# Performance work log

Hardware: AMD Instinct MI355X
Metric: run time of the kernel (lower is better)

The kernel has to match this reference:

```python
import jax, jax.numpy as jnp
import numpy as np

B, P_ATT, F, E, D, A, O, V, L = 128, 36, 2048, 1024, 1024, 1024, 512, 10000, 20


def setup_inputs() -> dict:
    key = jax.random.key(0)
    ks = jax.random.split(key, 20)
    g = lambda i, shape, s=0.02: jax.random.normal(ks[i], shape, jnp.float32) * s
    return {
        "img_att": g(0, (B, P_ATT, F), 1.0),
        "img_fc": g(1, (B, 1, F), 1.0),
        "encoded_captions": jax.random.randint(ks[2], (B, L), 0, V),
        "caption_lengths": jax.random.randint(ks[3], (B, 1), 2, L + 1),
        "emb": jax.random.uniform(ks[4], (V, E), jnp.float32, -0.1, 0.1),
        "Wfa": g(5, (A, F)), "bfa": jnp.zeros((A,), jnp.float32),
        "Wd1": g(6, (A, D)), "bd1": jnp.zeros((A,), jnp.float32),
        "Wd2": g(7, (A, D)), "bd2": jnp.zeros((A,), jnp.float32),
        "Wfull": g(8, (1, A)), "bfull": jnp.zeros((1,), jnp.float32),
        "Wlang": g(9, (O, D)), "blang": jnp.zeros((O,), jnp.float32),
        "Watt": g(10, (O, D)), "batt": jnp.zeros((O,), jnp.float32),
        "Wout": g(11, (V, 2 * O)), "bout": jnp.zeros((V,), jnp.float32),
        "Wll_ih": g(12, (4 * D, E + D + F)), "Wll_hh": g(13, (4 * D, D)), "bll": jnp.zeros((4 * D,), jnp.float32),
        "Wal_ih": g(14, (4 * D, F)), "Wal_hh": g(15, (4 * D, D)), "bal": jnp.zeros((4 * D,), jnp.float32),
        "Wfc": g(16, (V, D)), "bfc": jnp.zeros((V,), jnp.float32),
    }


def _lstm_cell(x, h, c, Wih, Whh, b):
    # torch LSTMCell: gates ordered i, f, g, o; b = b_ih + b_hh
    gates = x @ Wih.T + h @ Whh.T + b
    i, f, g, o = jnp.split(gates, 4, axis=-1)
    c_new = jax.nn.sigmoid(f) * c + jax.nn.sigmoid(i) * jnp.tanh(g)
    h_new = jax.nn.sigmoid(o) * jnp.tanh(c_new)
    return h_new, c_new


def reference(img_att, img_fc, encoded_captions, caption_lengths, emb,
              Wfa, bfa, Wd1, bd1, Wd2, bd2, Wfull, bfull,
              Wlang, blang, Watt, batt, Wout, bout,
              Wll_ih, Wll_hh, bll, Wal_ih, Wal_hh, bal, Wfc, bfc):
    lengths = caption_lengths[:, 0]
    sort_ind = jnp.argsort(-lengths)  # stable descending sort by length
    lengths = lengths[sort_ind]
    image_features = jnp.concatenate([img_att, img_fc], axis=1)[sort_ind]  # (B, P, F)
    image_fc = img_fc[sort_ind, 0]  # (B, F)
    enc_caps = encoded_captions[sort_ind]
    embeddings = emb[enc_caps]  # (B, L, E)
    decode_lengths = lengths - 1
    T = enc_caps.shape[1] - 1
    Bsz = image_features.shape[0]
    Ddim = Wll_hh.shape[1]

    # attention key projection of image features is time-invariant: precompute
    att1 = jnp.einsum('bpf,af->bpa', image_features, Wfa) + bfa  # (B, P, A)

    def step(carry, x_t):
        h1, c1, h2, c2 = carry
        emb_t, t = x_t
        active = (t < decode_lengths)[:, None]  # (B, 1): rows beyond batch_size_t in torch
        x1 = jnp.concatenate([emb_t, h2, image_fc], axis=-1)
        h1n, c1n = _lstm_cell(x1, h1, c1, Wll_ih, Wll_hh, bll)
        preds1 = h1n @ Wfc.T + bfc  # dropout is identity in eval
        e = jax.nn.relu(att1 + (h1n @ Wd1.T + bd1)[:, None, :] + (h2 @ Wd2.T + bd2)[:, None, :])
        scores = jnp.einsum('bpa,a->bp', e, Wfull[0]) + bfull[0]
        alpha = jax.nn.softmax(scores, axis=1)
        awe = jnp.einsum('bpf,bp->bf', image_features, alpha)
        h2n, c2n = _lstm_cell(awe, h2, c2, Wal_ih, Wal_hh, bal)
        hid = jax.nn.relu(jnp.concatenate([h1n @ Wlang.T + blang, h2n @ Watt.T + batt], axis=-1))
        out = hid @ Wout.T + bout
        h1 = jnp.where(active, h1n, h1); c1 = jnp.where(active, c1n, c1)
        h2 = jnp.where(active, h2n, h2); c2 = jnp.where(active, c2n, c2)
        ys = (jnp.where(active, out, 0.0), jnp.where(active, preds1, 0.0), jnp.where(active, alpha, 0.0))
        return (h1, c1, h2, c2), ys

    init = tuple(jnp.zeros((Bsz, Ddim), image_features.dtype) for _ in range(4))
    xs = (jnp.swapaxes(embeddings[:, :T], 0, 1), jnp.arange(T))
    _, (preds, preds1, alphas) = jax.lax.scan(step, init, xs)
    predictions = jnp.swapaxes(preds, 0, 1)      # (B, T, V)
    predictions_1 = jnp.swapaxes(preds1, 0, 1)   # (B, T, V)
    alphas = jnp.swapaxes(alphas, 0, 1)          # (B, T, P)
    return predictions, predictions_1, enc_caps, decode_lengths, alphas, sort_ind
```

## Files before the change

### kernel.cpp

```cpp
#include <hip/hip_runtime.h>
#include <math.h>

#define BATCH 128
#define PATT 36
#define P_TOT 37
#define FDIM 2048
#define EDIM 1024
#define DDIM 1024
#define ADIM 1024
#define VOCAB 10000
#define LCAP 20
#define TSTEPS 19

typedef __attribute__((ext_vector_type(8))) short bf16x8v;
typedef __attribute__((ext_vector_type(4))) float f32x4v;

__device__ __forceinline__ ushort f2bf(float f) {
  unsigned u = __float_as_uint(f);
  unsigned r = (u + 0x7fffu + ((u >> 16) & 1u)) >> 16;
  return (ushort)r;
}
__device__ __forceinline__ float bf2f(ushort u) {
  return __uint_as_float(((unsigned)u) << 16);
}

__device__ __forceinline__ void gld16(const ushort* g, ushort* l) {
  __builtin_amdgcn_global_load_lds(
      (const __attribute__((address_space(1))) unsigned int*)(g),
      (__attribute__((address_space(3))) unsigned int*)(l), 16, 0, 0);
}

__global__ void setup_kernel(const int* __restrict__ cap_len,
                             const int* __restrict__ enc_caps,
                             int* __restrict__ sort_ind, int* __restrict__ dec_len,
                             float* __restrict__ out_enc, float* __restrict__ out_dec,
                             float* __restrict__ out_si) {
  __shared__ int s_len[BATCH];
  __shared__ int s_ind[BATCH];
  int tid = threadIdx.x;
  if (tid < BATCH) s_len[tid] = cap_len[tid];
  __syncthreads();
  if (tid < BATCH) {
    int key = s_len[tid];
    int pos = 0;
#pragma unroll 8
    for (int j = 0; j < BATCH; ++j) {
      int lj = s_len[j];
      pos += (lj > key) || (lj == key && j < tid);
    }
    s_ind[pos] = tid;
  }
  __syncthreads();
  for (int i = threadIdx.x; i < BATCH; i += blockDim.x) {
    int si = s_ind[i];
    sort_ind[i] = si;
    int dl = s_len[si] - 1;
    dec_len[i] = dl;
    out_dec[i] = (float)dl;
    out_si[i] = (float)si;
  }
  for (int i = threadIdx.x; i < BATCH * LCAP; i += blockDim.x) {
    int b = i / LCAP, l = i - b * LCAP;
    out_enc[i] = (float)enc_caps[s_ind[b] * LCAP + l];
  }
}

struct Seg { const float* src; ushort* dst; unsigned n; };
struct SegTab { Seg s[11]; };

__global__ __launch_bounds__(256) void convert_kernel(SegTab tab) {
  Seg sg = tab.s[blockIdx.y];
  unsigned i0 = (blockIdx.x * 256u + threadIdx.x) * 8u;
  if (i0 >= sg.n) return;
  float4 f0 = *(const float4*)(sg.src + i0);
  float4 f1 = *(const float4*)(sg.src + i0 + 4);
  ushort r[8];
  r[0] = f2bf(f0.x); r[1] = f2bf(f0.y); r[2] = f2bf(f0.z); r[3] = f2bf(f0.w);
  r[4] = f2bf(f1.x); r[5] = f2bf(f1.y); r[6] = f2bf(f1.z); r[7] = f2bf(f1.w);
  *(uint4*)(sg.dst + i0) = *(uint4*)r;
}

__global__ __launch_bounds__(256) void img_cat_kernel(const float* __restrict__ img_att,
                                                      const float* __restrict__ img_fc,
                                                      ushort* __restrict__ img_cat) {
  int b = blockIdx.x, p = blockIdx.y;
  const float* src = (p < PATT) ? img_att + ((size_t)b * PATT + p) * FDIM
                                : img_fc + (size_t)b * FDIM;
  ushort* dst = img_cat + ((size_t)b * P_TOT + p) * FDIM;
  int i0 = threadIdx.x * 8;
  float4 f0 = *(const float4*)(src + i0);
  float4 f1 = *(const float4*)(src + i0 + 4);
  ushort r[8];
  r[0] = f2bf(f0.x); r[1] = f2bf(f0.y); r[2] = f2bf(f0.z); r[3] = f2bf(f0.w);
  r[4] = f2bf(f1.x); r[5] = f2bf(f1.y); r[6] = f2bf(f1.z); r[7] = f2bf(f1.w);
  *(uint4*)(dst + i0) = *(uint4*)r;
}

__global__ __launch_bounds__(256) void gemm_mfma_kernel(
    const ushort* __restrict__ X, int ldx,
    const ushort* __restrict__ Wa, int Ka,
    const ushort* __restrict__ Wb, int Kb,
    const float* __restrict__ bias1, const float* __restrict__ bias2,
    float* __restrict__ C, ushort* __restrict__ Cb, long ldc,
    int N, int relu, const int* __restrict__ dec_len, int t)
{
  __shared__ __align__(16) ushort s_A[3][128][64];
  __shared__ __align__(16) ushort s_B[3][64][64];

  const int tid = threadIdx.x;
  const int lane = tid & 63;
  const int wv = tid >> 6;
  const int wm = wv >> 1;
  const int wn = wv & 1;
  const int q = lane >> 4;
  const int c16 = lane & 15;

  const int bm = blockIdx.x * 128;
  const int bn = blockIdx.y * 64;
  const int K = Ka + Kb;
  const int nt = K >> 6;

  f32x4v acc[4][2];
#pragma unroll
  for (int i = 0; i < 4; ++i)
#pragma unroll
    for (int j = 0; j < 2; ++j) acc[i][j] = (f32x4v){0.f, 0.f, 0.f, 0.f};

  auto stage = [&](int s, int tch) {
    const int k0 = tch << 6;
#pragma unroll
    for (int i = 0; i < 4; ++i) {
      int gid = i * 256 + tid;
      int r = gid >> 3, gp = gid & 7;
      int gl = gp ^ (r & 7);
      const ushort* src = X + (size_t)(bm + r) * ldx + k0 + gl * 8;
      gld16(src, &s_A[s][r][gp * 8]);
    }
#pragma unroll
    for (int i = 0; i < 2; ++i) {
      int gid = i * 256 + tid;
      int r = gid >> 3, gp = gid & 7;
      int gl = gp ^ (r & 7);
      int gn = bn + r;
      if (gn >= N) gn = N - 1;
      int kk = k0 + gl * 8;
      const ushort* src = (kk < Ka) ? Wa + (size_t)gn * Ka + kk
                                    : Wb + (size_t)gn * Kb + (kk - Ka);
      gld16(src, &s_B[s][r][gp * 8]);
    }
  };

  stage(0, 0);
  if (nt > 1) {
    stage(1, 1);
    asm volatile("s_waitcnt vmcnt(6)" ::: "memory");
  } else {
    asm volatile("s_waitcnt vmcnt(0)" ::: "memory");
  }
  __builtin_amdgcn_s_barrier();
  asm volatile("" ::: "memory");

  int cur = 0;
  for (int k = 0; k < nt; ++k) {
    if (k + 2 < nt) {
      int nxt = cur + 2; if (nxt >= 3) nxt -= 3;
      stage(nxt, k + 2);
    }
#pragma unroll
    for (int ks = 0; ks < 2; ++ks) {
      const int gpa = ((ks << 2) + q) ^ (c16 & 7);
      bf16x8v a[4], b[2];
#pragma unroll
      for (int mf = 0; mf < 4; ++mf)
        a[mf] = *(const bf16x8v*)&s_A[cur][wm * 64 + mf * 16 + c16][gpa * 8];
#pragma unroll
      for (int nf = 0; nf < 2; ++nf)
        b[nf] = *(const bf16x8v*)&s_B[cur][wn * 32 + nf * 16 + c16][gpa * 8];
#pragma unroll
      for (int mf = 0; mf < 4; ++mf)
#pragma unroll
        for (int nf = 0; nf < 2; ++nf)
          acc[mf][nf] = __builtin_amdgcn_mfma_f32_16x16x32_bf16(a[mf], b[nf], acc[mf][nf], 0, 0, 0);
    }
    if (k + 2 < nt) asm volatile("s_waitcnt vmcnt(6)" ::: "memory");
    else            asm volatile("s_waitcnt vmcnt(0)" ::: "memory");
    __builtin_amdgcn_s_barrier();
    asm volatile("" ::: "memory");
    cur = (cur == 2) ? 0 : cur + 1;
  }

#pragma unroll
  for (int nf = 0; nf < 2; ++nf) {
    int gcol = bn + wn * 32 + nf * 16 + c16;
    if (gcol >= N) continue;
    float bsum = bias1[gcol] + (bias2 ? bias2[gcol] : 0.f);
#pragma unroll
    for (int mf = 0; mf < 4; ++mf) {
#pragma unroll
      for (int rr = 0; rr < 4; ++rr) {
        int grow = bm + wm * 64 + mf * 16 + q * 4 + rr;
        float v = acc[mf][nf][rr] + bsum;
        if (relu) v = fmaxf(v, 0.f);
        if (dec_len && !(t < dec_len[grow])) v = 0.f;
        if (C)  C[(size_t)grow * ldc + gcol] = v;
        if (Cb) Cb[(size_t)grow * ldc + gcol] = f2bf(v);
      }
    }
  }
}

__global__ void build_x1_kernel(const float* __restrict__ emb, const int* __restrict__ enc_caps,
                                const int* __restrict__ sort_ind, const ushort* __restrict__ img_cat,
                                const ushort* __restrict__ h1bf, const ushort* __restrict__ h2bf,
                                ushort* __restrict__ x1cat, int t) {
  int b = blockIdx.x;
  int si = sort_ind[b];
  int cap = enc_caps[si * LCAP + t];
  const float* erow = emb + (size_t)cap * EDIM;
  const ushort* fcrow = img_cat + ((size_t)si * P_TOT + PATT) * FDIM;
  ushort* dst = x1cat + (size_t)b * 5120;
  for (int k = threadIdx.x; k < EDIM; k += 256) dst[k] = f2bf(erow[k]);
  for (int k = threadIdx.x; k < DDIM; k += 256) dst[EDIM + k] = h2bf[b * DDIM + k];
  for (int k = threadIdx.x; k < FDIM; k += 256) dst[EDIM + DDIM + k] = fcrow[k];
  for (int k = threadIdx.x; k < DDIM; k += 256) dst[EDIM + DDIM + FDIM + k] = h1bf[b * DDIM + k];
}

__global__ void lstm_cell_kernel(const float* __restrict__ gates,
                                 float* __restrict__ h, float* __restrict__ c,
                                 const int* __restrict__ dec_len, int t,
                                 ushort* __restrict__ hbf,
                                 ushort* __restrict__ hcat, const ushort* __restrict__ h_other_bf) {
  int idx = blockIdx.x * blockDim.x + threadIdx.x;
  int b = idx >> 10, j = idx & 1023;
  const float* g = gates + (size_t)b * 4096;
  float iv = 1.f / (1.f + expf(-g[j]));
  float fv = 1.f / (1.f + expf(-g[1024 + j]));
  float gv = tanhf(g[2048 + j]);
  float ov = 1.f / (1.f + expf(-g[3072 + j]));
  float cn = fv * c[idx] + iv * gv;
  float hn = ov * tanhf(cn);
  bool act = t < dec_len[b];
  float hw = act ? hn : h[idx];
  float cw = act ? cn : c[idx];
  h[idx] = hw; c[idx] = cw;
  hbf[idx] = f2bf(hw);
  if (hcat) {
    hcat[b * 2048 + j] = f2bf(hw);
    hcat[b * 2048 + 1024 + j] = h_other_bf[idx];
  }
}

__global__ __launch_bounds__(256) void attention_kernel(
    const ushort* __restrict__ att1, const float* __restrict__ d12,
    const float* __restrict__ Wfull, const float* __restrict__ bfull,
    const ushort* __restrict__ img_cat,
    const int* __restrict__ sort_ind, const int* __restrict__ dec_len,
    ushort* __restrict__ x2cat, const ushort* __restrict__ h2bf,
    float* __restrict__ out_alphas, int t) {
  int b = blockIdx.x;
  int si = sort_ind[b];
  __shared__ float dsh[ADIM];
  __shared__ float sc[P_TOT];
  __shared__ float al[P_TOT + 3];
  int tid = threadIdx.x;
  for (int k = tid; k < ADIM; k += 256) dsh[k] = d12[b * ADIM + k];
  __syncthreads();
  int wave = tid >> 6, lane = tid & 63;
  for (int p = wave; p < P_TOT; p += 4) {
    const ushort* arow = att1 + ((size_t)si * P_TOT + p) * ADIM;
    float s = 0.f;
    for (int k = lane * 4; k < ADIM; k += 256) {
      ushort4 av = *(const ushort4*)&arow[k];
      float e0 = fmaxf(bf2f(av.x) + dsh[k + 0], 0.f);
      float e1 = fmaxf(bf2f(av.y) + dsh[k + 1], 0.f);
      float e2 = fmaxf(bf2f(av.z) + dsh[k + 2], 0.f);
      float e3 = fmaxf(bf2f(av.w) + dsh[k + 3], 0.f);
      s += e0 * Wfull[k] + e1 * Wfull[k + 1] + e2 * Wfull[k + 2] + e3 * Wfull[k + 3];
    }
    for (int off = 32; off; off >>= 1) s += __shfl_down(s, off, 64);
    if (lane == 0) sc[p] = s + bfull[0];
  }
  __syncthreads();
  if (tid == 0) {
    float mx = sc[0];
    for (int p = 1; p < P_TOT; ++p) mx = fmaxf(mx, sc[p]);
    float sum = 0.f;
    for (int p = 0; p < P_TOT; ++p) { float e = expf(sc[p] - mx); al[p] = e; sum += e; }
    float inv = 1.f / sum;
    for (int p = 0; p < P_TOT; ++p) al[p] *= inv;
  }
  __syncthreads();
  bool act = t < dec_len[b];
  if (tid < P_TOT)
    out_alphas[((size_t)b * TSTEPS + t) * P_TOT + tid] = act ? al[tid] : 0.f;
  for (int f0 = tid * 4; f0 < FDIM; f0 += 1024) {
    float a0 = 0.f, a1 = 0.f, a2 = 0.f, a3 = 0.f;
#pragma unroll 4
    for (int p = 0; p < P_TOT; ++p) {
      ushort4 iv = *(const ushort4*)&img_cat[((size_t)si * P_TOT + p) * FDIM + f0];
      float w = al[p];
      a0 += w * bf2f(iv.x); a1 += w * bf2f(iv.y);
      a2 += w * bf2f(iv.z); a3 += w * bf2f(iv.w);
    }
    ushort* dst = x2cat + (size_t)b * 3072 + f0;
    dst[0] = f2bf(a0); dst[1] = f2bf(a1); dst[2] = f2bf(a2); dst[3] = f2bf(a3);
  }
  for (int j = tid; j < DDIM; j += 256)
    x2cat[(size_t)b * 3072 + FDIM + j] = h2bf[b * DDIM + j];
}

extern "C" void kernel_launch(void* const* d_in, const int* in_sizes, int n_in,
                              void* d_out, int out_size, void* d_ws, size_t ws_size,
                              hipStream_t stream) {
  const float* img_att = (const float*)d_in[0];
  const float* img_fc  = (const float*)d_in[1];
  const int*   enc_caps= (const int*)d_in[2];
  const int*   cap_len = (const int*)d_in[3];
  const float* emb     = (const float*)d_in[4];
  const float* Wfa     = (const float*)d_in[5];
  const float* bfa     = (const float*)d_in[6];
  const float* Wd1     = (const float*)d_in[7];
  const float* bd1     = (const float*)d_in[8];
  const float* Wd2     = (const float*)d_in[9];
  const float* bd2     = (const float*)d_in[10];
  const float* Wfull   = (const float*)d_in[11];
  const float* bfull   = (const float*)d_in[12];
  const float* Wlang   = (const float*)d_in[13];
  const float* blang   = (const float*)d_in[14];
  const float* Watt    = (const float*)d_in[15];
  const float* batt    = (const float*)d_in[16];
  const float* Wout    = (const float*)d_in[17];
  const float* bout    = (const float*)d_in[18];
  const float* Wll_ih  = (const float*)d_in[19];
  const float* Wll_hh  = (const float*)d_in[20];
  const float* bll     = (const float*)d_in[21];
  const float* Wal_ih  = (const float*)d_in[22];
  const float* Wal_hh  = (const float*)d_in[23];
  const float* bal     = (const float*)d_in[24];
  const float* Wfc     = (const float*)d_in[25];
  const float* bfc     = (const float*)d_in[26];

  int* sort_ind = (int*)d_ws;
  int* dec_len  = sort_ind + BATCH;
  float* fbase = (float*)d_ws + 256;
  const size_t BD = (size_t)BATCH * DDIM;
  float* h1    = fbase;
  float* c1    = h1 + BD;
  float* h2    = c1 + BD;
  float* c2    = h2 + BD;
  float* gates = c2 + BD;
  float* d12   = gates + (size_t)BATCH * 4096;
  ushort* ubase = (ushort*)(d12 + BD);
  ushort* h1bf   = ubase;
  ushort* h2bf   = h1bf + BD;
  ushort* x1cat  = h2bf + BD;
  ushort* hcat   = x1cat + (size_t)BATCH * 5120;
  ushort* x2cat  = hcat + (size_t)BATCH * 2048;
  ushort* hid_bf = x2cat + (size_t)BATCH * 3072;
  ushort* att1_bf= hid_bf + BD;
  ushort* img_cat= att1_bf + (size_t)BATCH * P_TOT * ADIM;
  ushort* wb     = img_cat + (size_t)BATCH * P_TOT * FDIM;
  ushort* Wfa_b  = wb;                 wb += (size_t)ADIM * FDIM;
  ushort* Wd1_b  = wb;                 wb += (size_t)ADIM * DDIM;
  ushort* Wd2_b  = wb;                 wb += (size_t)ADIM * DDIM;
  ushort* Wlang_b= wb;                 wb += (size_t)512 * DDIM;
  ushort* Watt_b = wb;                 wb += (size_t)512 * DDIM;
  ushort* Wout_b = wb;                 wb += (size_t)VOCAB * 1024;
  ushort* Wll_ih_b = wb;               wb += (size_t)4096 * 4096;
  ushort* Wll_hh_b = wb;               wb += (size_t)4096 * 1024;
  ushort* Wal_ih_b = wb;               wb += (size_t)4096 * 2048;
  ushort* Wal_hh_b = wb;               wb += (size_t)4096 * 1024;
  ushort* Wfc_b  = wb;                 wb += (size_t)VOCAB * 1024;

  float* out      = (float*)d_out;
  float* out_pred = out;
  float* out_pred1= out_pred  + (size_t)BATCH * TSTEPS * VOCAB;
  float* out_enc  = out_pred1 + (size_t)BATCH * TSTEPS * VOCAB;
  float* out_dec  = out_enc + (size_t)BATCH * LCAP;
  float* out_alph = out_dec + BATCH;
  float* out_si   = out_alph + (size_t)BATCH * TSTEPS * P_TOT;

  setup_kernel<<<1, 256, 0, stream>>>(cap_len, enc_caps, sort_ind, dec_len,
                                      out_enc, out_dec, out_si);
  hipMemsetAsync(h1, 0, 4 * BD * sizeof(float), stream);
  hipMemsetAsync(h1bf, 0, 2 * BD * sizeof(ushort), stream);

  SegTab tab;
  tab.s[0]  = {Wfa,    Wfa_b,    (unsigned)(ADIM * FDIM)};
  tab.s[1]  = {Wd1,    Wd1_b,    (unsigned)(ADIM * DDIM)};
  tab.s[2]  = {Wd2,    Wd2_b,    (unsigned)(ADIM * DDIM)};
  tab.s[3]  = {Wlang,  Wlang_b,  (unsigned)(512 * DDIM)};
  tab.s[4]  = {Watt,   Watt_b,   (unsigned)(512 * DDIM)};
  tab.s[5]  = {Wout,   Wout_b,   (unsigned)(VOCAB * 1024)};
  tab.s[6]  = {Wll_ih, Wll_ih_b, (unsigned)(4096 * 4096)};
  tab.s[7]  = {Wll_hh, Wll_hh_b, (unsigned)(4096 * 1024)};
  tab.s[8]  = {Wal_ih, Wal_ih_b, (unsigned)(4096 * 2048)};
  tab.s[9]  = {Wal_hh, Wal_hh_b, (unsigned)(4096 * 1024)};
  tab.s[10] = {Wfc,    Wfc_b,    (unsigned)(VOCAB * 1024)};
  convert_kernel<<<dim3(8192, 11), 256, 0, stream>>>(tab);

  img_cat_kernel<<<dim3(BATCH, P_TOT), 256, 0, stream>>>(img_att, img_fc, img_cat);

  gemm_mfma_kernel<<<dim3(37, 16), 256, 0, stream>>>(
      img_cat, FDIM, Wfa_b, FDIM, nullptr, 0, bfa, nullptr,
      nullptr, att1_bf, ADIM, ADIM, 0, nullptr, 0);

  const long ldo = (long)TSTEPS * VOCAB;
  for (int t = 0; t < TSTEPS; ++t) {
    build_x1_kernel<<<BATCH, 256, 0, stream>>>(emb, enc_caps, sort_ind, img_cat,
                                               h1bf, h2bf, x1cat, t);
    gemm_mfma_kernel<<<dim3(1, 64), 256, 0, stream>>>(
        x1cat, 5120, Wll_ih_b, 4096, Wll_hh_b, 1024, bll, nullptr,
        gates, nullptr, 4096, 4096, 0, nullptr, 0);
    lstm_cell_kernel<<<(BATCH * DDIM) / 256, 256, 0, stream>>>(
        gates, h1, c1, dec_len, t, h1bf, hcat, h2bf);
    gemm_mfma_kernel<<<dim3(1, 157), 256, 0, stream>>>(
        h1bf, 1024, Wfc_b, 1024, nullptr, 0, bfc, nullptr,
        out_pred1 + (size_t)t * VOCAB, nullptr, ldo, VOCAB, 0, dec_len, t);
    gemm_mfma_kernel<<<dim3(1, 16), 256, 0, stream>>>(
        hcat, 2048, Wd1_b, 1024, Wd2_b, 1024, bd1, bd2,
        d12, nullptr, 1024, 1024, 0, nullptr, 0);
    attention_kernel<<<BATCH, 256, 0, stream>>>(
        att1_bf, d12, Wfull, bfull, img_cat, sort_ind, dec_len,
        x2cat, h2bf, out_alph, t);
    gemm_mfma_kernel<<<dim3(1, 64), 256, 0, stream>>>(
        x2cat, 3072, Wal_ih_b, 2048, Wal_hh_b, 1024, bal, nullptr,
        gates, nullptr, 4096, 4096, 0, nullptr, 0);
    lstm_cell_kernel<<<(BATCH * DDIM) / 256, 256, 0, stream>>>(
        gates, h2, c2, dec_len, t, h2bf, nullptr, nullptr);
    gemm_mfma_kernel<<<dim3(1, 8), 256, 0, stream>>>(
        h1bf, 1024, Wlang_b, 1024, nullptr, 0, blang, nullptr,
        nullptr, hid_bf, 1024, 512, 1, nullptr, 0);
    gemm_mfma_kernel<<<dim3(1, 8), 256, 0, stream>>>(
        h2bf, 1024, Watt_b, 1024, nullptr, 0, batt, nullptr,
        nullptr, hid_bf + 512, 1024, 512, 1, nullptr, 0);
    gemm_mfma_kernel<<<dim3(1, 157), 256, 0, stream>>>(
        hid_bf, 1024, Wout_b, 1024, nullptr, 0, bout, nullptr,
        out_pred + (size_t)t * VOCAB, nullptr, ldo, VOCAB, 0, dec_len, t);
  }
}
```

Measured before the change: 5.498 ms.

## Fuse LSTM cell into gate GEMM epilogue and gather GEMM inputs directly

Fuses the LSTM cell into the gate GEMM epilogue by interleaving the i,f,g,o rows of the LSTM weights and biases, so each 64-column tile holds all four gates for 16 hidden units. The concat-building kernels are removed: the GEMM A-loader gathers rows straight from the embedding, h, image features and awe buffers through per-row base pointers. The h buffers are double-buffered, the Wlang and Watt GEMMs are merged into one launch, and the pipeline depth goes from three to four stages. This cuts kernel launches and intermediate gate and concat traffic per step, at the cost of more LDS and a more complex kernel.

```diff
diff --git a/kernel.cpp b/kernel.cpp
--- a/kernel.cpp
+++ b/kernel.cpp
@@ -30,11 +30,19 @@
       (__attribute__((address_space(3))) unsigned int*)(l), 16, 0, 0);
 }
 
+__device__ __forceinline__ void wait_stages(int cnt) {
+  if (cnt >= 2)      asm volatile("s_waitcnt vmcnt(12)" ::: "memory");
+  else if (cnt == 1) asm volatile("s_waitcnt vmcnt(6)"  ::: "memory");
+  else               asm volatile("s_waitcnt vmcnt(0)"  ::: "memory");
+}
+
 __global__ void setup_kernel(const int* __restrict__ cap_len,
                              const int* __restrict__ enc_caps,
                              int* __restrict__ sort_ind, int* __restrict__ dec_len,
                              float* __restrict__ out_enc, float* __restrict__ out_dec,
-                             float* __restrict__ out_si) {
+                             float* __restrict__ out_si,
+                             const float* __restrict__ bll, const float* __restrict__ bal,
+                             float* __restrict__ bll_p, float* __restrict__ bal_p) {
   __shared__ int s_len[BATCH];
   __shared__ int s_ind[BATCH];
   int tid = threadIdx.x;
@@ -51,7 +59,7 @@
     s_ind[pos] = tid;
   }
   __syncthreads();
-  for (int i = threadIdx.x; i < BATCH; i += blockDim.x) {
+  for (int i = tid; i < BATCH; i += blockDim.x) {
     int si = s_ind[i];
     sort_ind[i] = si;
     int dl = s_len[si] - 1;
@@ -59,14 +67,19 @@
     out_dec[i] = (float)dl;
     out_si[i] = (float)si;
   }
-  for (int i = threadIdx.x; i < BATCH * LCAP; i += blockDim.x) {
+  for (int i = tid; i < BATCH * LCAP; i += blockDim.x) {
     int b = i / LCAP, l = i - b * LCAP;
     out_enc[i] = (float)enc_caps[s_ind[b] * LCAP + l];
   }
-}
-
-struct Seg { const float* src; ushort* dst; unsigned n; };
-struct SegTab { Seg s[11]; };
+  for (int p = tid; p < 4096; p += blockDim.x) {
+    int src = (p & 3) * 1024 + (p >> 2);
+    bll_p[p] = bll[src];
+    bal_p[p] = bal[src];
+  }
+}
+
+struct Seg { const float* src; ushort* dst; unsigned n; unsigned rl; };
+struct SegTab { Seg s[12]; };
 
 __global__ __launch_bounds__(256) void convert_kernel(SegTab tab) {
   Seg sg = tab.s[blockIdx.y];
@@ -77,7 +90,13 @@
   ushort r[8];
   r[0] = f2bf(f0.x); r[1] = f2bf(f0.y); r[2] = f2bf(f0.z); r[3] = f2bf(f0.w);
   r[4] = f2bf(f1.x); r[5] = f2bf(f1.y); r[6] = f2bf(f1.z); r[7] = f2bf(f1.w);
-  *(uint4*)(sg.dst + i0) = *(uint4*)r;
+  unsigned dsti = i0;
+  if (sg.rl) {
+    unsigned rw = i0 >> sg.rl;
+    unsigned col = i0 & ((1u << sg.rl) - 1u);
+    dsti = ((4u * (rw & 1023u) + (rw >> 10)) << sg.rl) + col;
+  }
+  *(uint4*)(sg.dst + dsti) = *(uint4*)r;
 }
 
 __global__ __launch_bounds__(256) void img_cat_kernel(const float* __restrict__ img_att,
@@ -96,16 +115,38 @@
   *(uint4*)(dst + i0) = *(uint4*)r;
 }
 
+struct GatherX {
+  const ushort* p[4];
+  int kend[4];
+  int rstride[4];
+  int mode[4];
+  int nseg;
+};
+
 __global__ __launch_bounds__(256) void gemm_mfma_kernel(
-    const ushort* __restrict__ X, int ldx,
-    const ushort* __restrict__ Wa, int Ka,
+    const ushort* __restrict__ Xp, int ldx,
+    const ushort* __restrict__ Wap, int Ka,
     const ushort* __restrict__ Wb, int Kb,
-    const float* __restrict__ bias1, const float* __restrict__ bias2,
-    float* __restrict__ C, ushort* __restrict__ Cb, long ldc,
-    int N, int relu, const int* __restrict__ dec_len, int t)
+    const float* __restrict__ bias1p, const float* __restrict__ bias2,
+    float* __restrict__ C, ushort* __restrict__ Cbp, long ldc,
+    int N, int relu, const int* __restrict__ dec_len, int t,
+    GatherX gx, const int* __restrict__ sort_ind_g, const int* __restrict__ enc_caps_g,
+    float* __restrict__ lstm_h, float* __restrict__ lstm_c, ushort* __restrict__ lstm_hbf,
+    const ushort* __restrict__ Xalt, const ushort* __restrict__ Waalt,
+    const float* __restrict__ biasalt, ushort* __restrict__ Cbalt, int ysplit)
 {
-  __shared__ __align__(16) ushort s_A[3][128][64];
-  __shared__ __align__(16) ushort s_B[3][64][64];
+  __shared__ __align__(16) ushort s_A[4][128][64];
+  __shared__ __align__(16) ushort s_B[4][64][64];
+  __shared__ const ushort* s_rowbase[4][128];
+
+  const ushort* X = Xp;
+  const ushort* Wa = Wap;
+  const float* bias1 = bias1p;
+  ushort* Cb = Cbp;
+  int by = blockIdx.y;
+  if (ysplit && by >= ysplit) {
+    X = Xalt; Wa = Waalt; bias1 = biasalt; Cb = Cbalt; by -= ysplit;
+  }
 
   const int tid = threadIdx.x;
   const int lane = tid & 63;
@@ -116,9 +157,25 @@
   const int c16 = lane & 15;
 
   const int bm = blockIdx.x * 128;
-  const int bn = blockIdx.y * 64;
+  const int bn = by * 64;
   const int K = Ka + Kb;
   const int nt = K >> 6;
+  const bool gather = gx.nseg > 0;
+
+  if (gather) {
+    for (int r = tid; r < 128; r += 256) {
+      int si = sort_ind_g[r];
+      for (int sgi = 0; sgi < gx.nseg; ++sgi) {
+        const ushort* bp;
+        int m = gx.mode[sgi];
+        if (m == 0)      bp = gx.p[sgi] + (size_t)r * gx.rstride[sgi];
+        else if (m == 1) bp = gx.p[sgi] + (size_t)enc_caps_g[si * LCAP + t] * gx.rstride[sgi];
+        else             bp = gx.p[sgi] + ((size_t)si * P_TOT + PATT) * gx.rstride[sgi];
+        s_rowbase[sgi][r] = bp;
+      }
+    }
+    __syncthreads();
+  }
 
   f32x4v acc[4][2];
 #pragma unroll
@@ -128,19 +185,30 @@
 
   auto stage = [&](int s, int tch) {
     const int k0 = tch << 6;
-#pragma unroll
-    for (int i = 0; i < 4; ++i) {
-      int gid = i * 256 + tid;
-      int r = gid >> 3, gp = gid & 7;
-      int gl = gp ^ (r & 7);
-      const ushort* src = X + (size_t)(bm + r) * ldx + k0 + gl * 8;
-      gld16(src, &s_A[s][r][gp * 8]);
+    if (gather) {
+      int sg = 0;
+#pragma unroll
+      for (int z = 0; z < 3; ++z)
+        if (sg + 1 < gx.nseg && k0 >= gx.kend[sg]) ++sg;
+      const int kst = sg ? gx.kend[sg - 1] : 0;
+#pragma unroll
+      for (int i = 0; i < 4; ++i) {
+        int gid = i * 256 + tid;
+        int r = gid >> 3, gp = gid & 7, gl = gp ^ (r & 7);
+        gld16(s_rowbase[sg][r] + (k0 - kst) + gl * 8, &s_A[s][r][gp * 8]);
+      }
+    } else {
+#pragma unroll
+      for (int i = 0; i < 4; ++i) {
+        int gid = i * 256 + tid;
+        int r = gid >> 3, gp = gid & 7, gl = gp ^ (r & 7);
+        gld16(X + (size_t)(bm + r) * ldx + k0 + gl * 8, &s_A[s][r][gp * 8]);
+      }
     }
 #pragma unroll
     for (int i = 0; i < 2; ++i) {
       int gid = i * 256 + tid;
-      int r = gid >> 3, gp = gid & 7;
-      int gl = gp ^ (r & 7);
+      int r = gid >> 3, gp = gid & 7, gl = gp ^ (r & 7);
       int gn = bn + r;
       if (gn >= N) gn = N - 1;
       int kk = k0 + gl * 8;
@@ -150,43 +218,81 @@
     }
   };
 
-  stage(0, 0);
-  if (nt > 1) {
-    stage(1, 1);
-    asm volatile("s_waitcnt vmcnt(6)" ::: "memory");
-  } else {
-    asm volatile("s_waitcnt vmcnt(0)" ::: "memory");
-  }
+  auto compute = [&](int s) {
+#pragma unroll
+    for (int ks = 0; ks < 2; ++ks) {
+      const int gpa = ((ks << 2) + q) ^ (c16 & 7);
+      bf16x8v a[4], b2[2];
+#pragma unroll
+      for (int mf = 0; mf < 4; ++mf)
+        a[mf] = *(const bf16x8v*)&s_A[s][wm * 64 + mf * 16 + c16][gpa * 8];
+#pragma unroll
+      for (int nf = 0; nf < 2; ++nf)
+        b2[nf] = *(const bf16x8v*)&s_B[s][wn * 32 + nf * 16 + c16][gpa * 8];
+#pragma unroll
+      for (int mf = 0; mf < 4; ++mf)
+#pragma unroll
+        for (int nf = 0; nf < 2; ++nf)
+          acc[mf][nf] = __builtin_amdgcn_mfma_f32_16x16x32_bf16(a[mf], b2[nf], acc[mf][nf], 0, 0, 0);
+    }
+  };
+
+  const int pre = nt < 3 ? nt : 3;
+  for (int s2 = 0; s2 < pre; ++s2) stage(s2, s2);
+  wait_stages(pre - 1);
   __builtin_amdgcn_s_barrier();
   asm volatile("" ::: "memory");
 
-  int cur = 0;
   for (int k = 0; k < nt; ++k) {
-    if (k + 2 < nt) {
-      int nxt = cur + 2; if (nxt >= 3) nxt -= 3;
-      stage(nxt, k + 2);
-    }
-#pragma unroll
-    for (int ks = 0; ks < 2; ++ks) {
-      const int gpa = ((ks << 2) + q) ^ (c16 & 7);
-      bf16x8v a[4], b[2];
-#pragma unroll
-      for (int mf = 0; mf < 4; ++mf)
-        a[mf] = *(const bf16x8v*)&s_A[cur][wm * 64 + mf * 16 + c16][gpa * 8];
-#pragma unroll
-      for (int nf = 0; nf < 2; ++nf)
-        b[nf] = *(const bf16x8v*)&s_B[cur][wn * 32 + nf * 16 + c16][gpa * 8];
-#pragma unroll
-      for (int mf = 0; mf < 4; ++mf)
-#pragma unroll
-        for (int nf = 0; nf < 2; ++nf)
-          acc[mf][nf] = __builtin_amdgcn_mfma_f32_16x16x32_bf16(a[mf], b[nf], acc[mf][nf], 0, 0, 0);
-    }
-    if (k + 2 < nt) asm volatile("s_waitcnt vmcnt(6)" ::: "memory");
-    else            asm volatile("s_waitcnt vmcnt(0)" ::: "memory");
+    if (k + 3 < nt) stage((k + 3) & 3, k + 3);
+    compute(k & 3);
+    int li = (k + 3 < nt) ? (k + 3) : (nt - 1);
+    int cnt = li - (k + 1);
+    if (cnt < 0) cnt = 0;
+    wait_stages(cnt);
     __builtin_amdgcn_s_barrier();
     asm volatile("" ::: "memory");
-    cur = (cur == 2) ? 0 : cur + 1;
+  }
+
+  if (lstm_h) {
+    float* ft = (float*)&s_A[0][0][0];
+#pragma unroll
+    for (int nf = 0; nf < 2; ++nf) {
+      int lc = wn * 32 + nf * 16 + c16;
+      float bsum = bias1[bn + lc];
+#pragma unroll
+      for (int mf = 0; mf < 4; ++mf)
+#pragma unroll
+        for (int rr = 0; rr < 4; ++rr) {
+          int lr = wm * 64 + mf * 16 + q * 4 + rr;
+          ft[lr * 64 + lc] = acc[mf][nf][rr] + bsum;
+        }
+    }
+    __syncthreads();
+    const int j0 = bn >> 2;
+#pragma unroll
+    for (int uu = 0; uu < 8; ++uu) {
+      int u = uu * 256 + tid;
+      int b = u >> 4, jj = u & 15;
+      float gi_ = ft[b * 64 + jj * 4 + 0];
+      float gf_ = ft[b * 64 + jj * 4 + 1];
+      float gg_ = ft[b * 64 + jj * 4 + 2];
+      float go_ = ft[b * 64 + jj * 4 + 3];
+      float siv = 1.f / (1.f + expf(-gi_));
+      float sfv = 1.f / (1.f + expf(-gf_));
+      float sov = 1.f / (1.f + expf(-go_));
+      int idx = b * 1024 + j0 + jj;
+      float co = lstm_c[idx];
+      float cn = sfv * co + siv * tanhf(gg_);
+      float hn = sov * tanhf(cn);
+      bool act = t < dec_len[b];
+      float hw = act ? hn : lstm_h[idx];
+      float cw = act ? cn : co;
+      lstm_h[idx] = hw;
+      lstm_c[idx] = cw;
+      lstm_hbf[idx] = f2bf(hw);
+    }
+    return;
   }
 
 #pragma unroll
@@ -209,54 +315,12 @@
   }
 }
 
-__global__ void build_x1_kernel(const float* __restrict__ emb, const int* __restrict__ enc_caps,
-                                const int* __restrict__ sort_ind, const ushort* __restrict__ img_cat,
-                                const ushort* __restrict__ h1bf, const ushort* __restrict__ h2bf,
-                                ushort* __restrict__ x1cat, int t) {
-  int b = blockIdx.x;
-  int si = sort_ind[b];
-  int cap = enc_caps[si * LCAP + t];
-  const float* erow = emb + (size_t)cap * EDIM;
-  const ushort* fcrow = img_cat + ((size_t)si * P_TOT + PATT) * FDIM;
-  ushort* dst = x1cat + (size_t)b * 5120;
-  for (int k = threadIdx.x; k < EDIM; k += 256) dst[k] = f2bf(erow[k]);
-  for (int k = threadIdx.x; k < DDIM; k += 256) dst[EDIM + k] = h2bf[b * DDIM + k];
-  for (int k = threadIdx.x; k < FDIM; k += 256) dst[EDIM + DDIM + k] = fcrow[k];
-  for (int k = threadIdx.x; k < DDIM; k += 256) dst[EDIM + DDIM + FDIM + k] = h1bf[b * DDIM + k];
-}
-
-__global__ void lstm_cell_kernel(const float* __restrict__ gates,
-                                 float* __restrict__ h, float* __restrict__ c,
-                                 const int* __restrict__ dec_len, int t,
-                                 ushort* __restrict__ hbf,
-                                 ushort* __restrict__ hcat, const ushort* __restrict__ h_other_bf) {
-  int idx = blockIdx.x * blockDim.x + threadIdx.x;
-  int b = idx >> 10, j = idx & 1023;
-  const float* g = gates + (size_t)b * 4096;
-  float iv = 1.f / (1.f + expf(-g[j]));
-  float fv = 1.f / (1.f + expf(-g[1024 + j]));
-  float gv = tanhf(g[2048 + j]);
-  float ov = 1.f / (1.f + expf(-g[3072 + j]));
-  float cn = fv * c[idx] + iv * gv;
-  float hn = ov * tanhf(cn);
-  bool act = t < dec_len[b];
-  float hw = act ? hn : h[idx];
-  float cw = act ? cn : c[idx];
-  h[idx] = hw; c[idx] = cw;
-  hbf[idx] = f2bf(hw);
-  if (hcat) {
-    hcat[b * 2048 + j] = f2bf(hw);
-    hcat[b * 2048 + 1024 + j] = h_other_bf[idx];
-  }
-}
-
 __global__ __launch_bounds__(256) void attention_kernel(
     const ushort* __restrict__ att1, const float* __restrict__ d12,
     const float* __restrict__ Wfull, const float* __restrict__ bfull,
     const ushort* __restrict__ img_cat,
     const int* __restrict__ sort_ind, const int* __restrict__ dec_len,
-    ushort* __restrict__ x2cat, const ushort* __restrict__ h2bf,
-    float* __restrict__ out_alphas, int t) {
+    ushort* __restrict__ x2awe, float* __restrict__ out_alphas, int t) {
   int b = blockIdx.x;
   int si = sort_ind[b];
   __shared__ float dsh[ADIM];
@@ -302,11 +366,9 @@
       a0 += w * bf2f(iv.x); a1 += w * bf2f(iv.y);
       a2 += w * bf2f(iv.z); a3 += w * bf2f(iv.w);
     }
-    ushort* dst = x2cat + (size_t)b * 3072 + f0;
+    ushort* dst = x2awe + (size_t)b * 2048 + f0;
     dst[0] = f2bf(a0); dst[1] = f2bf(a1); dst[2] = f2bf(a2); dst[3] = f2bf(a3);
   }
-  for (int j = tid; j < DDIM; j += 256)
-    x2cat[(size_t)b * 3072 + FDIM + j] = h2bf[b * DDIM + j];
 }
 
 extern "C" void kernel_launch(void* const* d_in, const int* in_sizes, int n_in,
@@ -342,24 +404,26 @@
 
   int* sort_ind = (int*)d_ws;
   int* dec_len  = sort_ind + BATCH;
+  const size_t BD = (size_t)BATCH * DDIM;
   float* fbase = (float*)d_ws + 256;
-  const size_t BD = (size_t)BATCH * DDIM;
   float* h1    = fbase;
   float* c1    = h1 + BD;
   float* h2    = c1 + BD;
   float* c2    = h2 + BD;
-  float* gates = c2 + BD;
-  float* d12   = gates + (size_t)BATCH * 4096;
-  ushort* ubase = (ushort*)(d12 + BD);
-  ushort* h1bf   = ubase;
-  ushort* h2bf   = h1bf + BD;
-  ushort* x1cat  = h2bf + BD;
-  ushort* hcat   = x1cat + (size_t)BATCH * 5120;
-  ushort* x2cat  = hcat + (size_t)BATCH * 2048;
-  ushort* hid_bf = x2cat + (size_t)BATCH * 3072;
-  ushort* att1_bf= hid_bf + BD;
-  ushort* img_cat= att1_bf + (size_t)BATCH * P_TOT * ADIM;
-  ushort* wb     = img_cat + (size_t)BATCH * P_TOT * FDIM;
+  float* d12   = c2 + BD;
+  float* bll_p = d12 + BD;
+  float* bal_p = bll_p + 4096;
+  ushort* ubase = (ushort*)(bal_p + 4096);
+  ushort* h1bfA = ubase;
+  ushort* h1bfB = h1bfA + BD;
+  ushort* h2bfA = h1bfB + BD;
+  ushort* h2bfB = h2bfA + BD;
+  ushort* x2awe = h2bfB + BD;
+  ushort* hid_bf = x2awe + (size_t)BATCH * 2048;
+  ushort* att1_bf = hid_bf + BD;
+  ushort* img_cat = att1_bf + (size_t)BATCH * P_TOT * ADIM;
+  ushort* emb_bf  = img_cat + (size_t)BATCH * P_TOT * FDIM;
+  ushort* wb     = emb_bf + (size_t)VOCAB * EDIM;
   ushort* Wfa_b  = wb;                 wb += (size_t)ADIM * FDIM;
   ushort* Wd1_b  = wb;                 wb += (size_t)ADIM * DDIM;
   ushort* Wd2_b  = wb;                 wb += (size_t)ADIM * DDIM;
@@ -381,61 +445,95 @@
   float* out_si   = out_alph + (size_t)BATCH * TSTEPS * P_TOT;
 
   setup_kernel<<<1, 256, 0, stream>>>(cap_len, enc_caps, sort_ind, dec_len,
-                                      out_enc, out_dec, out_si);
+                                      out_enc, out_dec, out_si, bll, bal, bll_p, bal_p);
   hipMemsetAsync(h1, 0, 4 * BD * sizeof(float), stream);
-  hipMemsetAsync(h1bf, 0, 2 * BD * sizeof(ushort), stream);
+  hipMemsetAsync(h1bfA, 0, 4 * BD * sizeof(ushort), stream);
 
   SegTab tab;
-  tab.s[0]  = {Wfa,    Wfa_b,    (unsigned)(ADIM * FDIM)};
-  tab.s[1]  = {Wd1,    Wd1_b,    (unsigned)(ADIM * DDIM)};
-  tab.s[2]  = {Wd2,    Wd2_b,    (unsigned)(ADIM * DDIM)};
-  tab.s[3]  = {Wlang,  Wlang_b,  (unsigned)(512 * DDIM)};
-  tab.s[4]  = {Watt,   Watt_b,   (unsigned)(512 * DDIM)};
-  tab.s[5]  = {Wout,   Wout_b,   (unsigned)(VOCAB * 1024)};
-  tab.s[6]  = {Wll_ih, Wll_ih_b, (unsigned)(4096 * 4096)};
-  tab.s[7]  = {Wll_hh, Wll_hh_b, (unsigned)(4096 * 1024)};
-  tab.s[8]  = {Wal_ih, Wal_ih_b, (unsigned)(4096 * 2048)};
-  tab.s[9]  = {Wal_hh, Wal_hh_b, (unsigned)(4096 * 1024)};
-  tab.s[10] = {Wfc,    Wfc_b,    (unsigned)(VOCAB * 1024)};
-  convert_kernel<<<dim3(8192, 11), 256, 0, stream>>>(tab);
+  tab.s[0]  = {Wfa,    Wfa_b,    (unsigned)(ADIM * FDIM),  0};
+  tab.s[1]  = {Wd1,    Wd1_b,    (unsigned)(ADIM * DDIM),  0};
+  tab.s[2]  = {Wd2,    Wd2_b,    (unsigned)(ADIM * DDIM),  0};
+  tab.s[3]  = {Wlang,  Wlang_b,  (unsigned)(512 * DDIM),   0};
+  tab.s[4]  = {Watt,   Watt_b,   (unsigned)(512 * DDIM),   0};
+  tab.s[5]  = {Wout,   Wout_b,   (unsigned)(VOCAB * 1024), 0};
+  tab.s[6]  = {Wfc,    Wfc_b,    (unsigned)(VOCAB * 1024), 0};
+  tab.s[7]  = {Wll_ih, Wll_ih_b, (unsigned)(4096 * 4096),  12};
+  tab.s[8]  = {Wll_hh, Wll_hh_b, (unsigned)(4096 * 1024),  10};
+  tab.s[9]  = {Wal_ih, Wal_ih_b, (unsigned)(4096 * 2048),  11};
+  tab.s[10] = {Wal_hh, Wal_hh_b, (unsigned)(4096 * 1024),  10};
+  tab.s[11] = {emb,    emb_bf,   (unsigned)(VOCAB * EDIM), 0};
+  convert_kernel<<<dim3(8192, 12), 256, 0, stream>>>(tab);
 
   img_cat_kernel<<<dim3(BATCH, P_TOT), 256, 0, stream>>>(img_att, img_fc, img_cat);
+
+  GatherX g0 = {};
 
   gemm_mfma_kernel<<<dim3(37, 16), 256, 0, stream>>>(
       img_cat, FDIM, Wfa_b, FDIM, nullptr, 0, bfa, nullptr,
-      nullptr, att1_bf, ADIM, ADIM, 0, nullptr, 0);
+      nullptr, att1_bf, ADIM, ADIM, 0, nullptr, 0,
+      g0, sort_ind, enc_caps, nullptr, nullptr, nullptr,
+      nullptr, nullptr, nullptr, nullptr, 0);
 
   const long ldo = (long)TSTEPS * VOCAB;
+  ushort *h1r = h1bfA, *h1w = h1bfB, *h2r = h2bfA, *h2w = h2bfB;
+
   for (int t = 0; t < TSTEPS; ++t) {
-    build_x1_kernel<<<BATCH, 256, 0, stream>>>(emb, enc_caps, sort_ind, img_cat,
-                                               h1bf, h2bf, x1cat, t);
+    GatherX g1;
+    g1.p[0] = emb_bf;  g1.kend[0] = 1024; g1.rstride[0] = EDIM; g1.mode[0] = 1;
+    g1.p[1] = h2r;     g1.kend[1] = 2048; g1.rstride[1] = DDIM; g1.mode[1] = 0;
+    g1.p[2] = img_cat; g1.kend[2] = 4096; g1.rstride[2] = FDIM; g1.mode[2] = 2;
+    g1.p[3] = h1r;     g1.kend[3] = 5120; g1.rstride[3] = DDIM; g1.mode[3] = 0;
+    g1.nseg = 4;
     gemm_mfma_kernel<<<dim3(1, 64), 256, 0, stream>>>(
-        x1cat, 5120, Wll_ih_b, 4096, Wll_hh_b, 1024, bll, nullptr,
-        gates, nullptr, 4096, 4096, 0, nullptr, 0);
-    lstm_cell_kernel<<<(BATCH * DDIM) / 256, 256, 0, stream>>>(
-        gates, h1, c1, dec_len, t, h1bf, hcat, h2bf);
+        nullptr, 0, Wll_ih_b, 4096, Wll_hh_b, 1024, bll_p, nullptr,
+        nullptr, nullptr, 0, 4096, 0, dec_len, t,
+        g1, sort_ind, enc_caps, h1, c1, h1w,
+        nullptr, nullptr, nullptr, nullptr, 0);
+
     gemm_mfma_kernel<<<dim3(1, 157), 256, 0, stream>>>(
-        h1bf, 1024, Wfc_b, 1024, nullptr, 0, bfc, nullptr,
-        out_pred1 + (size_t)t * VOCAB, nullptr, ldo, VOCAB, 0, dec_len, t);
+        h1w, 1024, Wfc_b, 1024, nullptr, 0, bfc, nullptr,
+        out_pred1 + (size_t)t * VOCAB, nullptr, ldo, VOCAB, 0, dec_len, t,
+        g0, sort_ind, enc_caps, nullptr, nullptr, nullptr,
+        nullptr, nullptr, nullptr, nullptr, 0);
+
+    GatherX g2;
+    g2.p[0] = h1w; g2.kend[0] = 1024; g2.rstride[0] = DDIM; g2.mode[0] = 0;
+    g2.p[1] = h2r; g2.kend[1] = 2048; g2.rstride[1] = DDIM; g2.mode[1] = 0;
+    g2.nseg = 2;
     gemm_mfma_kernel<<<dim3(1, 16), 256, 0, stream>>>(
-        hcat, 2048, Wd1_b, 1024, Wd2_b, 1024, bd1, bd2,
-        d12, nullptr, 1024, 1024, 0, nullptr, 0);
+        nullptr, 0, Wd1_b, 1024, Wd2_b, 1024, bd1, bd2,
+        d12, nullptr, 1024, 1024, 0, nullptr, 0,
+        g2, sort_ind, enc_caps, nullptr, nullptr, nullptr,
+        nullptr, nullptr, nullptr, nullptr, 0);
+
     attention_kernel<<<BATCH, 256, 0, stream>>>(
         att1_bf, d12, Wfull, bfull, img_cat, sort_ind, dec_len,
-        x2cat, h2bf, out_alph, t);
+        x2awe, out_alph, t);
+
+    GatherX g3;
+    g3.p[0] = x2awe; g3.kend[0] = 2048; g3.rstride[0] = 2048; g3.mode[0] = 0;
+    g3.p[1] = h2r;   g3.kend[1] = 3072; g3.rstride[1] = DDIM; g3.mode[1] = 0;
+    g3.nseg = 2;
     gemm_mfma_kernel<<<dim3(1, 64), 256, 0, stream>>>(
-        x2cat, 3072, Wal_ih_b, 2048, Wal_hh_b, 1024, bal, nullptr,
-        gates, nullptr, 4096, 4096, 0, nullptr, 0);
-    lstm_cell_kernel<<<(BATCH * DDIM) / 256, 256, 0, stream>>>(
-        gates, h2, c2, dec_len, t, h2bf, nullptr, nullptr);
-    gemm_mfma_kernel<<<dim3(1, 8), 256, 0, stream>>>(
-        h1bf, 1024, Wlang_b, 1024, nullptr, 0, blang, nullptr,
-        nullptr, hid_bf, 1024, 512, 1, nullptr, 0);
-    gemm_mfma_kernel<<<dim3(1, 8), 256, 0, stream>>>(
-        h2bf, 1024, Watt_b, 1024, nullptr, 0, batt, nullptr,
-        nullptr, hid_bf + 512, 1024, 512, 1, nullptr, 0);
+        nullptr, 0, Wal_ih_b, 2048, Wal_hh_b, 1024, bal_p, nullptr,
+        nullptr, nullptr, 0, 4096, 0, dec_len, t,
+        g3, sort_ind, enc_caps, h2, c2, h2w,
+        nullptr, nullptr, nullptr, nullptr, 0);
+
+    gemm_mfma_kernel<<<dim3(1, 16), 256, 0, stream>>>(
+        h1w, 1024, Wlang_b, 1024, nullptr, 0, blang, nullptr,
+        nullptr, hid_bf, 1024, 512, 1, nullptr, 0,
+        g0, sort_ind, enc_caps, nullptr, nullptr, nullptr,
+        h2w, Watt_b, batt, hid_bf + 512, 8);
+
     gemm_mfma_kernel<<<dim3(1, 157), 256, 0, stream>>>(
         hid_bf, 1024, Wout_b, 1024, nullptr, 0, bout, nullptr,
-        out_pred + (size_t)t * VOCAB, nullptr, ldo, VOCAB, 0, dec_len, t);
-  }
-}
+        out_pred + (size_t)t * VOCAB, nullptr, ldo, VOCAB, 0, dec_len, t,
+        g0, sort_ind, enc_caps, nullptr, nullptr, nullptr,
+        nullptr, nullptr, nullptr, nullptr, 0);
+
+    ushort* tmp;
+    tmp = h1r; h1r = h1w; h1w = tmp;
+    tmp = h2r; h2r = h2w; h2w = tmp;
+  }
+}
```

New measurement: 5.665 ms. 3.0% more time.
